# Optimization experiments

Hardware: AMD Instinct MI355X
Metric: run time of the kernel (lower is better)

## Reference

```python
import jax, jax.numpy as jnp
import numpy as np

GROUPS = 256   # == planes (default groups=None -> planes)
NODE_NUM = 32
EPS = 1e-5


def setup_inputs() -> dict:
    key = jax.random.key(0)
    ks = jax.random.split(key, 12)
    b, cin, planes, h, w = 4, 512, 256, 128, 128
    node_fea = planes // NODE_NUM  # 8
    inp = {
        "x": jax.random.normal(ks[0], (b, cin, h, w), jnp.float32),
        "Wt": jax.random.normal(ks[1], (planes, cin), jnp.float32) * 0.02,
        "Wp": jax.random.normal(ks[2], (planes, cin), jnp.float32) * 0.02,
        "Wg": jax.random.normal(ks[3], (planes, cin), jnp.float32) * 0.02,
        "Wz": jax.random.normal(ks[4], (cin,), jnp.float32) * 0.1,  # grouped 1x1 conv, 1 in-ch per group
        "W_adj": jax.random.normal(ks[5], (NODE_NUM, NODE_NUM), jnp.float32) * 0.1,
        "bn_adj_gamma": jnp.ones((NODE_NUM,), jnp.float32),
        "bn_adj_beta": jnp.zeros((NODE_NUM,), jnp.float32),
        "bn_adj_mean": jax.random.normal(ks[6], (NODE_NUM,), jnp.float32) * 0.1,
        "bn_adj_var": jax.random.uniform(ks[7], (NODE_NUM,), jnp.float32) + 0.5,
        "W_wg": jax.random.normal(ks[8], (node_fea, node_fea), jnp.float32) * 0.1,
        "bn_wg_gamma": jnp.ones((node_fea,), jnp.float32),
        "bn_wg_beta": jnp.zeros((node_fea,), jnp.float32),
        "bn_wg_mean": jax.random.normal(ks[9], (node_fea,), jnp.float32) * 0.1,
        "bn_wg_var": jax.random.uniform(ks[10], (node_fea,), jnp.float32) + 0.5,
        "gn_gamma": jnp.ones((cin,), jnp.float32),
        "gn_beta": jnp.zeros((cin,), jnp.float32),
    }
    return inp


def _bn1d_eval(z, mean, var, gamma, beta):
    # BatchNorm1d over channel dim 1 of [b, C, L], eval mode (running stats)
    inv = jax.lax.rsqrt(var + EPS)
    return (z - mean[:, None]) * (inv * gamma)[:, None] + beta[:, None]


def reference(x, Wt, Wp, Wg, Wz, W_adj, bn_adj_gamma, bn_adj_beta, bn_adj_mean,
              bn_adj_var, W_wg, bn_wg_gamma, bn_wg_beta, bn_wg_mean, bn_wg_var,
              gn_gamma, gn_beta):
    b, cin, h, w = x.shape
    # 1x1 convs t/p/g
    t = jnp.einsum('bihw,oi->bohw', x, Wt)
    p = jnp.einsum('bihw,oi->bohw', x, Wp)
    g = jnp.einsum('bihw,oi->bohw', x, Wg)
    planes = t.shape[1]
    node_fea = planes // NODE_NUM
    # per-group dot-product kernel: replaces the Python loop of tiny bmms.
    # _c = planes // GROUPS channels per group; att[b, gidx] = sum(p_g * g_g)
    att = jnp.sum((p * g).reshape(b, GROUPS, -1), axis=-1)  # [b, groups]
    # split(dim=1, node_num) + cat(dim=2): z_idt[b, i, k] = att[b, k*node_num + i]
    z_idt = att.reshape(b, GROUPS // NODE_NUM, NODE_NUM).transpose(0, 2, 1)  # [b, node_num, node_fea]
    # node-adjacency conv (Conv1d k=1 over node dim) + BN + ReLU + residual
    z = jnp.einsum('nm,bmf->bnf', W_adj, z_idt)
    z = _bn1d_eval(z, bn_adj_mean, bn_adj_var, bn_adj_gamma, bn_adj_beta)
    z = jax.nn.relu(z) + z_idt
    # feature conv on transposed layout + BN + ReLU
    z = z.transpose(0, 2, 1)  # [b, node_fea, node_num]
    z = jnp.einsum('fe,ben->bfn', W_wg, z)
    z = _bn1d_eval(z, bn_wg_mean, bn_wg_var, bn_wg_gamma, bn_wg_beta)
    z = jax.nn.relu(z).transpose(0, 2, 1)  # [b, node_num, node_fea]
    # reshape to per-channel scalars and gate t
    zvec = z.reshape(b, planes)[:, :, None, None]  # [b, planes, 1, 1]
    xg = zvec * t  # [b, planes, h, w]
    # grouped 1x1 conv z: groups=planes, 1 input ch / group, r=cin//planes out ch / group
    r = cin // planes
    y = Wz[None, :, None, None] * jnp.repeat(xg, r, axis=1)  # [b, cin, h, w]
    # GroupNorm(num_groups=GROUPS, num_channels=cin)
    yg = y.reshape(b, GROUPS, -1)  # each group: (cin//GROUPS)*h*w elements
    mean = yg.mean(axis=-1, keepdims=True)
    var = yg.var(axis=-1, keepdims=True)
    yn = ((yg - mean) * jax.lax.rsqrt(var + EPS)).reshape(b, cin, h, w)
    yn = yn * gn_gamma[None, :, None, None] + gn_beta[None, :, None, None]
    return yn + x
```

## Files before the change

### kernel.cpp

```cpp
#include <hip/hip_runtime.h>

#define HW 16384
#define CIN 512
#define PL 256
#define EPSF 1e-5f
#define SLO 0.0009765625f

using half8  = __attribute__((ext_vector_type(8))) _Float16;
using half4v = __attribute__((ext_vector_type(4))) _Float16;
using f32x4  = __attribute__((ext_vector_type(4))) float;

__device__ inline void gload_lds16(const void* g, void* l) {
  __builtin_amdgcn_global_load_lds((const __attribute__((address_space(1))) void*)g,
                                   (__attribute__((address_space(3))) void*)l, 16, 0, 0);
}

__global__ __launch_bounds__(256) void k_conv(const float* __restrict__ x,
                                              _Float16* __restrict__ Xh,
                                              _Float16* __restrict__ Xl,
                                              float* __restrict__ xsum) {
  __shared__ float ws4[4];
  int row = blockIdx.x;
  int tid = threadIdx.x;
  const float* xr = x + ((size_t)row << 14);
  _Float16* hr = Xh + ((size_t)row << 14);
  _Float16* lr = Xl + ((size_t)row << 14);
  float s = 0.f;
#pragma unroll
  for (int j = 0; j < 8; ++j) {
    int o = j * 2048 + tid * 8;
    float4 v0 = *reinterpret_cast<const float4*>(xr + o);
    float4 v1 = *reinterpret_cast<const float4*>(xr + o + 4);
    half8 h, l;
    h[0] = (_Float16)v0.x; h[1] = (_Float16)v0.y; h[2] = (_Float16)v0.z; h[3] = (_Float16)v0.w;
    h[4] = (_Float16)v1.x; h[5] = (_Float16)v1.y; h[6] = (_Float16)v1.z; h[7] = (_Float16)v1.w;
    l[0] = (_Float16)((v0.x - (float)h[0]) * 1024.f);
    l[1] = (_Float16)((v0.y - (float)h[1]) * 1024.f);
    l[2] = (_Float16)((v0.z - (float)h[2]) * 1024.f);
    l[3] = (_Float16)((v0.w - (float)h[3]) * 1024.f);
    l[4] = (_Float16)((v1.x - (float)h[4]) * 1024.f);
    l[5] = (_Float16)((v1.y - (float)h[5]) * 1024.f);
    l[6] = (_Float16)((v1.z - (float)h[6]) * 1024.f);
    l[7] = (_Float16)((v1.w - (float)h[7]) * 1024.f);
    *reinterpret_cast<half8*>(hr + o) = h;
    *reinterpret_cast<half8*>(lr + o) = l;
    s += v0.x + v0.y + v0.z + v0.w + v1.x + v1.y + v1.z + v1.w;
  }
#pragma unroll
  for (int m = 1; m < 64; m <<= 1) s += __shfl_xor(s, m);
  if ((tid & 63) == 0) ws4[tid >> 6] = s;
  __syncthreads();
  if (tid == 0) xsum[row] = ws4[0] + ws4[1] + ws4[2] + ws4[3];
}

__global__ __launch_bounds__(256, 4) void k_gx(const _Float16* __restrict__ Xh,
                                               const _Float16* __restrict__ Xl,
                                               float* __restrict__ GH,
                                               float* __restrict__ C1,
                                               _Float16* __restrict__ xT) {
  __shared__ char smem[32768];
  int tid = threadIdx.x;

  if (blockIdx.x < 832) {
    _Float16* lA = (_Float16*)smem;
    _Float16* lB = (_Float16*)(smem + 16384);
    int wg = blockIdx.x;
    int id = (wg & 7) * 104 + (wg >> 3);
    int b = id / 208;
    int rem = id % 208;
    int ks = rem / 26;
    int u = rem % 26;
    int chain, ti, tj;
    if (u < 10) {
      chain = 0;
      ti = 0;
      while ((ti + 1) * (ti + 2) / 2 <= u) ++ti;
      tj = u - ti * (ti + 1) / 2;
    } else {
      chain = 1;
      int t = u - 10;
      ti = t >> 2; tj = t & 3;
    }
    int wave = tid >> 6, lane = tid & 63, l15 = lane & 15, l4 = lane >> 4;
    int wr = wave >> 1, wc = wave & 1;
    const _Float16* Asrc = (chain ? Xl : Xh) + (size_t)b * CIN * HW;
    const _Float16* Bsrc = Xh + (size_t)b * CIN * HW;
    float* D = chain ? C1 : GH;

    int srow = lane >> 3;
    int sgran = (lane & 7) ^ (srow & 7);
    int kbase = ks << 11;
    const _Float16* gA[4];
    const _Float16* gB[4];
#pragma unroll
    for (int i = 0; i < 4; ++i) {
      int row = i * 32 + wave * 8 + srow;
      gA[i] = Asrc + (size_t)(ti * 128 + row) * HW + kbase + sgran * 8;
      gB[i] = Bsrc + (size_t)(tj * 128 + row) * HW + kbase + sgran * 8;
    }
    char* ldA = (char*)lA + wave * 1024;
    char* ldB = (char*)lB + wave * 1024;

    int adA[4][2], adB[4][2];
#pragma unroll
    for (int rf = 0; rf < 4; ++rf) {
      int r = wr * 64 + rf * 16 + l15;
#pragma unroll
      for (int ksub = 0; ksub < 2; ++ksub)
        adA[rf][ksub] = r * 128 + (((ksub * 4 + l4) ^ (r & 7)) << 4);
    }
#pragma unroll
    for (int cf = 0; cf < 4; ++cf) {
      int c = wc * 64 + cf * 16 + l15;
#pragma unroll
      for (int ksub = 0; ksub < 2; ++ksub)
        adB[cf][ksub] = c * 128 + (((ksub * 4 + l4) ^ (c & 7)) << 4);
    }

    f32x4 acc[4][4];
#pragma unroll
    for (int rf = 0; rf < 4; ++rf)
#pragma unroll
      for (int cf = 0; cf < 4; ++cf) acc[rf][cf] = f32x4{0.f, 0.f, 0.f, 0.f};

    for (int s = 0; s < 32; ++s) {
      int ko = s * 64;
#pragma unroll
      for (int i = 0; i < 4; ++i) {
        gload_lds16(gA[i] + ko, ldA + i * 4096);
        gload_lds16(gB[i] + ko, ldB + i * 4096);
      }
      __syncthreads();
#pragma unroll
      for (int ksub = 0; ksub < 2; ++ksub) {
        half8 af[4], bf[4];
#pragma unroll
        for (int rf = 0; rf < 4; ++rf)
          af[rf] = *reinterpret_cast<const half8*>((char*)lA + adA[rf][ksub]);
#pragma unroll
        for (int cf = 0; cf < 4; ++cf)
          bf[cf] = *reinterpret_cast<const half8*>((char*)lB + adB[cf][ksub]);
#pragma unroll
        for (int rf = 0; rf < 4; ++rf)
#pragma unroll
          for (int cf = 0; cf < 4; ++cf)
            acc[rf][cf] = __builtin_amdgcn_mfma_f32_16x16x32_f16(af[rf], bf[cf], acc[rf][cf], 0, 0, 0);
      }
      __syncthreads();
    }

    size_t bo = (size_t)b << 18;
#pragma unroll
    for (int rf = 0; rf < 4; ++rf)
#pragma unroll
      for (int cf = 0; cf < 4; ++cf)
#pragma unroll
        for (int r = 0; r < 4; ++r) {
          int i = ti * 128 + wr * 64 + rf * 16 + l4 * 4 + r;
          int j = tj * 128 + wc * 64 + cf * 16 + l15;
          atomicAdd(D + bo + ((size_t)i << 9) + j, acc[rf][cf][r]);
        }
  } else {
    _Float16* lds = (_Float16*)smem;
    int bid = blockIdx.x - 832;
    int hw0 = (bid & 255) << 6;
    int c0 = ((bid >> 8) & 7) << 6;
    int b = bid >> 11;
    int rl = tid >> 3, seg = tid & 7;
    const _Float16* hb = Xh + ((size_t)b << 23);
#pragma unroll
    for (int pass = 0; pass < 2; ++pass) {
      int cl = pass * 32 + rl;
      half8 v = *reinterpret_cast<const half8*>(hb + ((size_t)(c0 + cl) << 14) + hw0 + seg * 8);
#pragma unroll
      for (int e = 0; e < 8; ++e) lds[(seg * 8 + e) * 72 + cl] = v[e];
    }
    __syncthreads();
    _Float16* tb = xT + (((size_t)b << 14) + hw0) * CIN + c0;
#pragma unroll
    for (int pass = 0; pass < 2; ++pass) {
      int hwl = pass * 32 + rl;
      half8 o = *reinterpret_cast<const half8*>(&lds[hwl * 72 + seg * 8]);
      *reinterpret_cast<half8*>(tb + (size_t)hwl * CIN + seg * 8) = o;
    }
  }
}

__global__ __launch_bounds__(256) void k_sym(const float* __restrict__ GH,
                                             const float* __restrict__ C1,
                                             float* __restrict__ Gs) {
  __shared__ float T1[64 * 65];
  __shared__ float TG[64 * 65];
  int I = blockIdx.x, J = blockIdx.y, b = blockIdx.z;
  int i0 = I << 6, j0 = J << 6;
  bool upper = (I >> 1) >= (J >> 1);
  size_t bo = (size_t)b << 18;
  int tid = threadIdx.x;
  int r = tid >> 2, cs = (tid & 3) << 4;
#pragma unroll
  for (int u = 0; u < 16; u += 4) {
    size_t toff = bo + (((size_t)(j0 + r)) << 9) + i0 + cs + u;
    float4 v = *reinterpret_cast<const float4*>(C1 + toff);
    T1[r * 65 + cs + u + 0] = v.x; T1[r * 65 + cs + u + 1] = v.y;
    T1[r * 65 + cs + u + 2] = v.z; T1[r * 65 + cs + u + 3] = v.w;
    if (!upper) {
      float4 g = *reinterpret_cast<const float4*>(GH + toff);
      TG[r * 65 + cs + u + 0] = g.x; TG[r * 65 + cs + u + 1] = g.y;
      TG[r * 65 + cs + u + 2] = g.z; TG[r * 65 + cs + u + 3] = g.w;
    }
  }
  __syncthreads();
#pragma unroll
  for (int u = 0; u < 16; u += 4) {
    size_t off = bo + (((size_t)(i0 + r)) << 9) + j0 + cs + u;
    float4 c = *reinterpret_cast<const float4*>(C1 + off);
    float t0 = T1[(cs + u + 0) * 65 + r];
    float t1 = T1[(cs + u + 1) * 65 + r];
    float t2 = T1[(cs + u + 2) * 65 + r];
    float t3 = T1[(cs + u + 3) * 65 + r];
    float4 o;
    if (upper) {
      float4 h = *reinterpret_cast<const float4*>(GH + off);
      o.x = h.x + SLO * (c.x + t0);
      o.y = h.y + SLO * (c.y + t1);
      o.z = h.z + SLO * (c.z + t2);
      o.w = h.w + SLO * (c.w + t3);
    } else {
      o.x = TG[(cs + u + 0) * 65 + r] + SLO * (c.x + t0);
      o.y = TG[(cs + u + 1) * 65 + r] + SLO * (c.y + t1);
      o.z = TG[(cs + u + 2) * 65 + r] + SLO * (c.z + t2);
      o.w = TG[(cs + u + 3) * 65 + r] + SLO * (c.w + t3);
    }
    *reinterpret_cast<float4*>(Gs + off) = o;
  }
}

__global__ __launch_bounds__(256) void k_V(const float* __restrict__ Gs,
                                           const float* __restrict__ Wg,
                                           const float* __restrict__ Wt,
                                           float* __restrict__ V) {
  __shared__ float Gl[64 * 65];
  __shared__ float Wl[64 * 65];
  int it = blockIdx.x, ot = blockIdx.y, b = blockIdx.z;
  int i0 = it << 6, o0 = ot << 6;
  int tid = threadIdx.x;
  int srow = tid >> 2, sseg = (tid & 3) << 4;
  const float* gsb = Gs + ((size_t)b << 18);
  int orow = o0 + srow;
  const float* wrow = (orow < 256) ? (Wg + (size_t)orow * 512) : (Wt + (size_t)(orow - 256) * 512);
  float acc[4][4];
#pragma unroll
  for (int a = 0; a < 4; ++a)
#pragma unroll
    for (int c = 0; c < 4; ++c) acc[a][c] = 0.f;
  int oy = (tid >> 4) << 2, ix = (tid & 15) << 2;
  for (int jc = 0; jc < 512; jc += 64) {
    __syncthreads();
#pragma unroll
    for (int u = 0; u < 16; u += 4) {
      float4 g = *reinterpret_cast<const float4*>(gsb + ((size_t)(i0 + srow) << 9) + jc + sseg + u);
      float4 w = *reinterpret_cast<const float4*>(wrow + jc + sseg + u);
      Gl[srow * 65 + sseg + u + 0] = g.x; Gl[srow * 65 + sseg + u + 1] = g.y;
      Gl[srow * 65 + sseg + u + 2] = g.z; Gl[srow * 65 + sseg + u + 3] = g.w;
      Wl[srow * 65 + sseg + u + 0] = w.x; Wl[srow * 65 + sseg + u + 1] = w.y;
      Wl[srow * 65 + sseg + u + 2] = w.z; Wl[srow * 65 + sseg + u + 3] = w.w;
    }
    __syncthreads();
    for (int j = 0; j < 64; ++j) {
      float w0 = Wl[(oy + 0) * 65 + j], w1 = Wl[(oy + 1) * 65 + j];
      float w2 = Wl[(oy + 2) * 65 + j], w3 = Wl[(oy + 3) * 65 + j];
      float g0 = Gl[(ix + 0) * 65 + j], g1 = Gl[(ix + 1) * 65 + j];
      float g2 = Gl[(ix + 2) * 65 + j], g3 = Gl[(ix + 3) * 65 + j];
      acc[0][0] += w0 * g0; acc[0][1] += w0 * g1; acc[0][2] += w0 * g2; acc[0][3] += w0 * g3;
      acc[1][0] += w1 * g0; acc[1][1] += w1 * g1; acc[1][2] += w1 * g2; acc[1][3] += w1 * g3;
      acc[2][0] += w2 * g0; acc[2][1] += w2 * g1; acc[2][2] += w2 * g2; acc[2][3] += w2 * g3;
      acc[3][0] += w3 * g0; acc[3][1] += w3 * g1; acc[3][2] += w3 * g2; acc[3][3] += w3 * g3;
    }
  }
  float* vb = V + ((size_t)b << 18);
#pragma unroll
  for (int a = 0; a < 4; ++a) {
    float4 vv = {acc[a][0], acc[a][1], acc[a][2], acc[a][3]};
    *reinterpret_cast<float4*>(vb + ((size_t)(o0 + oy + a) << 9) + i0 + ix) = vv;
  }
}

__global__ __launch_bounds__(256) void k_red2(const float* __restrict__ V,
                                              const float* __restrict__ xsum,
                                              const float* __restrict__ Wp,
                                              const float* __restrict__ Wt,
                                              float* __restrict__ att,
                                              float* __restrict__ tsum,
                                              float* __restrict__ tsq) {
  int blk = blockIdx.x;
  int b = blk >> 4;
  int og = (blk & 15) << 4;
  int tid = threadIdx.x;
  int ol = tid >> 4, seg = tid & 15;
  int o = og + ol;
  const float* vg = V + ((size_t)b << 18) + ((size_t)o << 9) + seg * 32;
  const float* vt = V + ((size_t)b << 18) + ((size_t)(256 + o) << 9) + seg * 32;
  const float* wp = Wp + (size_t)o * 512 + seg * 32;
  const float* wt = Wt + (size_t)o * 512 + seg * 32;
  const float* xs = xsum + b * CIN + seg * 32;
  float sa = 0.f, sq = 0.f, sm = 0.f;
#pragma unroll
  for (int i = 0; i < 32; i += 4) {
    float4 a = *reinterpret_cast<const float4*>(vg + i);
    float4 p = *reinterpret_cast<const float4*>(wp + i);
    float4 c = *reinterpret_cast<const float4*>(vt + i);
    float4 t = *reinterpret_cast<const float4*>(wt + i);
    float4 s = *reinterpret_cast<const float4*>(xs + i);
    sa += a.x * p.x + a.y * p.y + a.z * p.z + a.w * p.w;
    sq += c.x * t.x + c.y * t.y + c.z * t.z + c.w * t.w;
    sm += t.x * s.x + t.y * s.y + t.z * s.z + t.w * s.w;
  }
#pragma unroll
  for (int m = 1; m < 16; m <<= 1) {
    sa += __shfl_xor(sa, m);
    sq += __shfl_xor(sq, m);
    sm += __shfl_xor(sm, m);
  }
  if (seg == 0) {
    att[b * PL + o] = sa;
    tsq[b * PL + o] = sq;
    tsum[b * PL + o] = sm;
  }
}

__global__ __launch_bounds__(1024) void k_graph(
    const float* __restrict__ att, const float* __restrict__ tsum, const float* __restrict__ tsq,
    const float* __restrict__ W_adj, const float* __restrict__ bnag, const float* __restrict__ bnab,
    const float* __restrict__ bnam, const float* __restrict__ bnav,
    const float* __restrict__ W_wg, const float* __restrict__ bwgg, const float* __restrict__ bwgb,
    const float* __restrict__ bwgm, const float* __restrict__ bwgv,
    const float* __restrict__ Wz, const float* __restrict__ gng, const float* __restrict__ gnb,
    float* __restrict__ sA, float* __restrict__ sB) {
  __shared__ float att_l[4 * 256];
  __shared__ float z_l[4 * 256];
  __shared__ float zv_l[4 * 256];
  int tid = threadIdx.x;
  att_l[tid] = att[tid];
  __syncthreads();
  int b = tid >> 8, r = tid & 255, i = r >> 3, k = r & 7;
  float z1 = 0.f;
#pragma unroll
  for (int m = 0; m < 32; ++m) z1 += W_adj[i * 32 + m] * att_l[b * 256 + k * 32 + m];
  float inv = rsqrtf(bnav[i] + EPSF);
  float z = (z1 - bnam[i]) * inv * bnag[i] + bnab[i];
  z = fmaxf(z, 0.f) + att_l[b * 256 + k * 32 + i];
  z_l[b * 256 + i * 8 + k] = z;
  __syncthreads();
  float z2 = 0.f;
#pragma unroll
  for (int e = 0; e < 8; ++e) z2 += W_wg[k * 8 + e] * z_l[b * 256 + i * 8 + e];
  float inv2 = rsqrtf(bwgv[k] + EPSF);
  z2 = (z2 - bwgm[k]) * inv2 * bwgg[k] + bwgb[k];
  zv_l[b * 256 + i * 8 + k] = fmaxf(z2, 0.f);
  __syncthreads();
  int g = r;
  float s = zv_l[b * 256 + g];
  float m1 = tsum[b * 256 + g] * (1.f / 16384.f);
  float m2 = tsq[b * 256 + g] * (1.f / 16384.f);
  float a0 = Wz[2 * g] * s, a1 = Wz[2 * g + 1] * s;
  float mu = 0.5f * (a0 + a1) * m1;
  float ey2 = 0.5f * (a0 * a0 + a1 * a1) * m2;
  float var = ey2 - mu * mu;
  float invg = rsqrtf(var + EPSF);
  int c = b * CIN + 2 * g;
  sA[c]     = a0 * invg * gng[2 * g];
  sA[c + 1] = a1 * invg * gng[2 * g + 1];
  sB[c]     = gnb[2 * g]     - mu * invg * gng[2 * g];
  sB[c + 1] = gnb[2 * g + 1] - mu * invg * gng[2 * g + 1];
}

__global__ __launch_bounds__(256) void k_M(const float* __restrict__ Wt,
                                           const float* __restrict__ sA,
                                           _Float16* __restrict__ M) {
  int idx = blockIdx.x * 256 + threadIdx.x;
  int k8 = idx & 63;
  int c = (idx >> 6) & 511;
  int b = idx >> 15;
  float s = sA[b * 512 + c];
  const float* wrow = Wt + ((size_t)(c >> 1) << 9) + k8 * 8;
  int kbase = k8 * 8;
  half8 h;
#pragma unroll
  for (int j = 0; j < 8; ++j) {
    float v = s * wrow[j] + ((kbase + j) == c ? 1.f : 0.f);
    h[j] = (_Float16)v;
  }
  *reinterpret_cast<half8*>(M + (((size_t)(b * 512 + c)) << 9) + kbase) = h;
}

__global__ __launch_bounds__(256, 4) void k_tout(const _Float16* __restrict__ xT,
                                                 const _Float16* __restrict__ M,
                                                 const float* __restrict__ sB,
                                                 float* __restrict__ out) {
  __shared__ _Float16 lA[128 * 32];
  __shared__ _Float16 lB[128 * 32];
  int wg = blockIdx.x;
  int id = (wg & 7) * 256 + (wg >> 3);
  int b = id >> 9;
  int rem = id & 511;
  int ct = rem >> 7;
  int ht = rem & 127;
  int tid = threadIdx.x;
  int wave = tid >> 6, lane = tid & 63, l15 = lane & 15, l4 = lane >> 4;
  int wr = wave >> 1, wc = wave & 1;
  const _Float16* Mb = M + ((size_t)b << 18);
  const _Float16* xTb = xT + (size_t)b * HW * CIN;

  int srow = lane >> 2;
  int gran = (lane & 3) ^ ((srow >> 1) & 3);
  const _Float16* gA[2];
  const _Float16* gB[2];
#pragma unroll
  for (int i = 0; i < 2; ++i) {
    int row = i * 64 + wave * 16 + srow;
    gA[i] = Mb + ((size_t)(ct * 128 + row) << 9) + gran * 8;
    gB[i] = xTb + ((size_t)(ht * 128 + row) << 9) + gran * 8;
  }
  char* ldA = (char*)lA + wave * 1024;
  char* ldB = (char*)lB + wave * 1024;

  int adA[4], adB[4];
#pragma unroll
  for (int rf = 0; rf < 4; ++rf) {
    int r = wr * 64 + rf * 16 + l15;
    adA[rf] = r * 64 + ((l4 ^ ((r >> 1) & 3)) << 4);
  }
#pragma unroll
  for (int cf = 0; cf < 4; ++cf) {
    int c = wc * 64 + cf * 16 + l15;
    adB[cf] = c * 64 + ((l4 ^ ((c >> 1) & 3)) << 4);
  }

  f32x4 acc[4][4];
#pragma unroll
  for (int rf = 0; rf < 4; ++rf)
#pragma unroll
    for (int cf = 0; cf < 4; ++cf) acc[rf][cf] = f32x4{0.f, 0.f, 0.f, 0.f};

  for (int s = 0; s < 16; ++s) {
    int ko = s * 32;
    gload_lds16(gA[0] + ko, ldA);
    gload_lds16(gA[1] + ko, ldA + 4096);
    gload_lds16(gB[0] + ko, ldB);
    gload_lds16(gB[1] + ko, ldB + 4096);
    __syncthreads();
    half8 af[4], bf[4];
#pragma unroll
    for (int rf = 0; rf < 4; ++rf) af[rf] = *reinterpret_cast<const half8*>((char*)lA + adA[rf]);
#pragma unroll
    for (int cf = 0; cf < 4; ++cf) bf[cf] = *reinterpret_cast<const half8*>((char*)lB + adB[cf]);
#pragma unroll
    for (int rf = 0; rf < 4; ++rf)
#pragma unroll
      for (int cf = 0; cf < 4; ++cf)
        acc[rf][cf] = __builtin_amdgcn_mfma_f32_16x16x32_f16(af[rf], bf[cf], acc[rf][cf], 0, 0, 0);
    __syncthreads();
  }

  size_t outb = ((size_t)b * CIN) << 14;
#pragma unroll
  for (int rf = 0; rf < 4; ++rf) {
#pragma unroll
    for (int r = 0; r < 4; ++r) {
      int c = ct * 128 + wr * 64 + rf * 16 + l4 * 4 + r;
      float bb = sB[b * CIN + c];
      size_t off = outb + ((size_t)c << 14) + ht * 128 + wc * 64 + l15;
#pragma unroll
      for (int cf = 0; cf < 4; ++cf)
        out[off + cf * 16] = acc[rf][cf][r] + bb;
    }
  }
}

extern "C" void kernel_launch(void* const* d_in, const int* in_sizes, int n_in,
                              void* d_out, int out_size, void* d_ws, size_t ws_size,
                              hipStream_t stream) {
  const float* x    = (const float*)d_in[0];
  const float* Wt   = (const float*)d_in[1];
  const float* Wp   = (const float*)d_in[2];
  const float* Wg   = (const float*)d_in[3];
  const float* Wz   = (const float*)d_in[4];
  const float* Wadj = (const float*)d_in[5];
  const float* bnag = (const float*)d_in[6];
  const float* bnab = (const float*)d_in[7];
  const float* bnam = (const float*)d_in[8];
  const float* bnav = (const float*)d_in[9];
  const float* Wwg  = (const float*)d_in[10];
  const float* bwgg = (const float*)d_in[11];
  const float* bwgb = (const float*)d_in[12];
  const float* bwgm = (const float*)d_in[13];
  const float* bwgv = (const float*)d_in[14];
  const float* gng  = (const float*)d_in[15];
  const float* gnb  = (const float*)d_in[16];

  char* ws = (char*)d_ws;
  _Float16* xT = (_Float16*)(ws);
  float* GH   = (float*)(ws + 67371008);
  float* C1   = (float*)(ws + 71565312);
  float* Gs   = (float*)(ws + 75759616);
  float* V    = (float*)(ws + 79953920);
  float* xsum = (float*)(ws + 84148224);
  float* att  = (float*)(ws + 84156416);
  float* tsum = (float*)(ws + 84160512);
  float* tsq  = (float*)(ws + 84164608);
  float* sA   = (float*)(ws + 84168704);
  float* sB   = (float*)(ws + 84176896);
  if (ws_size < (size_t)84185088) return;
  _Float16* M = (_Float16*)GH;

  _Float16* Xh = (_Float16*)((char*)d_out);
  _Float16* Xl = (_Float16*)((char*)d_out + 67108864);
  float* out = (float*)d_out;

  hipMemsetAsync(GH, 0, 8388608, stream);
  k_conv<<<dim3(2048), dim3(256), 0, stream>>>(x, Xh, Xl, xsum);
  k_gx<<<dim3(9024), dim3(256), 0, stream>>>(Xh, Xl, GH, C1, xT);
  k_sym<<<dim3(8, 8, 4), dim3(256), 0, stream>>>(GH, C1, Gs);
  k_V<<<dim3(8, 8, 4), dim3(256), 0, stream>>>(Gs, Wg, Wt, V);
  k_red2<<<dim3(64), dim3(256), 0, stream>>>(V, xsum, Wp, Wt, att, tsum, tsq);
  k_graph<<<dim3(1), dim3(1024), 0, stream>>>(att, tsum, tsq, Wadj, bnag, bnab, bnam, bnav,
                                              Wwg, bwgg, bwgb, bwgm, bwgv, Wz, gng, gnb, sA, sB);
  k_M<<<dim3(512), dim3(256), 0, stream>>>(Wt, sA, M);
  k_tout<<<dim3(2048), dim3(256), 0, stream>>>(xT, M, sB, out);
}
```

Measured before the change: 263.4 us.

## Double K-step depth in k_tout GEMM and swizzle LDS transpose writes

The k_tout GEMM now stages a 64-wide K slice per iteration instead of 32. That halves the number of main-loop iterations and barrier pairs, and the LDS swizzle is reworked to an 8-granule XOR pattern. Separately, the xT transpose path in the conv kernel XOR-swizzles its LDS layout to reduce bank conflicts on scattered half writes. The costs are doubled LDS per block for k_tout, which may lower occupancy under the 4-blocks launch bound, and more address arithmetic.

```diff
diff --git a/kernel.cpp b/kernel.cpp
--- a/kernel.cpp
+++ b/kernel.cpp
@@ -171,16 +171,21 @@
 #pragma unroll
     for (int pass = 0; pass < 2; ++pass) {
       int cl = pass * 32 + rl;
+      int chunk = cl >> 3, wi = cl & 7;
       half8 v = *reinterpret_cast<const half8*>(hb + ((size_t)(c0 + cl) << 14) + hw0 + seg * 8);
 #pragma unroll
-      for (int e = 0; e < 8; ++e) lds[(seg * 8 + e) * 72 + cl] = v[e];
+      for (int e = 0; e < 8; ++e) {
+        int r = seg * 8 + e;
+        lds[r * 72 + ((chunk ^ ((r >> 3) & 7)) << 3) + wi] = v[e];
+      }
     }
     __syncthreads();
     _Float16* tb = xT + (((size_t)b << 14) + hw0) * CIN + c0;
 #pragma unroll
     for (int pass = 0; pass < 2; ++pass) {
       int hwl = pass * 32 + rl;
-      half8 o = *reinterpret_cast<const half8*>(&lds[hwl * 72 + seg * 8]);
+      int chp = seg ^ ((hwl >> 3) & 7);
+      half8 o = *reinterpret_cast<const half8*>(&lds[hwl * 72 + (chp << 3)]);
       *reinterpret_cast<half8*>(tb + (size_t)hwl * CIN + seg * 8) = o;
     }
   }
@@ -397,8 +402,8 @@
                                                  const _Float16* __restrict__ M,
                                                  const float* __restrict__ sB,
                                                  float* __restrict__ out) {
-  __shared__ _Float16 lA[128 * 32];
-  __shared__ _Float16 lB[128 * 32];
+  __shared__ _Float16 lA[128 * 64];
+  __shared__ _Float16 lB[128 * 64];
   int wg = blockIdx.x;
   int id = (wg & 7) * 256 + (wg >> 3);
   int b = id >> 9;
@@ -411,29 +416,33 @@
   const _Float16* Mb = M + ((size_t)b << 18);
   const _Float16* xTb = xT + (size_t)b * HW * CIN;
 
-  int srow = lane >> 2;
-  int gran = (lane & 3) ^ ((srow >> 1) & 3);
-  const _Float16* gA[2];
-  const _Float16* gB[2];
-#pragma unroll
-  for (int i = 0; i < 2; ++i) {
-    int row = i * 64 + wave * 16 + srow;
-    gA[i] = Mb + ((size_t)(ct * 128 + row) << 9) + gran * 8;
-    gB[i] = xTb + ((size_t)(ht * 128 + row) << 9) + gran * 8;
+  int srow = lane >> 3;
+  int sgran = (lane & 7) ^ (srow & 7);
+  const _Float16* gA[4];
+  const _Float16* gB[4];
+#pragma unroll
+  for (int i = 0; i < 4; ++i) {
+    int row = i * 32 + wave * 8 + srow;
+    gA[i] = Mb + ((size_t)(ct * 128 + row) << 9) + sgran * 8;
+    gB[i] = xTb + ((size_t)(ht * 128 + row) << 9) + sgran * 8;
   }
   char* ldA = (char*)lA + wave * 1024;
   char* ldB = (char*)lB + wave * 1024;
 
-  int adA[4], adB[4];
+  int adA[4][2], adB[4][2];
 #pragma unroll
   for (int rf = 0; rf < 4; ++rf) {
     int r = wr * 64 + rf * 16 + l15;
-    adA[rf] = r * 64 + ((l4 ^ ((r >> 1) & 3)) << 4);
+#pragma unroll
+    for (int ksub = 0; ksub < 2; ++ksub)
+      adA[rf][ksub] = r * 128 + (((ksub * 4 + l4) ^ (r & 7)) << 4);
   }
 #pragma unroll
   for (int cf = 0; cf < 4; ++cf) {
     int c = wc * 64 + cf * 16 + l15;
-    adB[cf] = c * 64 + ((l4 ^ ((c >> 1) & 3)) << 4);
+#pragma unroll
+    for (int ksub = 0; ksub < 2; ++ksub)
+      adB[cf][ksub] = c * 128 + (((ksub * 4 + l4) ^ (c & 7)) << 4);
   }
 
   f32x4 acc[4][4];
@@ -442,23 +451,29 @@
 #pragma unroll
     for (int cf = 0; cf < 4; ++cf) acc[rf][cf] = f32x4{0.f, 0.f, 0.f, 0.f};
 
-  for (int s = 0; s < 16; ++s) {
-    int ko = s * 32;
-    gload_lds16(gA[0] + ko, ldA);
-    gload_lds16(gA[1] + ko, ldA + 4096);
-    gload_lds16(gB[0] + ko, ldB);
-    gload_lds16(gB[1] + ko, ldB + 4096);
+  for (int s = 0; s < 8; ++s) {
+    int ko = s * 64;
+#pragma unroll
+    for (int i = 0; i < 4; ++i) {
+      gload_lds16(gA[i] + ko, ldA + i * 4096);
+      gload_lds16(gB[i] + ko, ldB + i * 4096);
+    }
     __syncthreads();
-    half8 af[4], bf[4];
-#pragma unroll
-    for (int rf = 0; rf < 4; ++rf) af[rf] = *reinterpret_cast<const half8*>((char*)lA + adA[rf]);
-#pragma unroll
-    for (int cf = 0; cf < 4; ++cf) bf[cf] = *reinterpret_cast<const half8*>((char*)lB + adB[cf]);
-#pragma unroll
-    for (int rf = 0; rf < 4; ++rf)
+#pragma unroll
+    for (int ksub = 0; ksub < 2; ++ksub) {
+      half8 af[4], bf[4];
+#pragma unroll
+      for (int rf = 0; rf < 4; ++rf)
+        af[rf] = *reinterpret_cast<const half8*>((char*)lA + adA[rf][ksub]);
 #pragma unroll
       for (int cf = 0; cf < 4; ++cf)
-        acc[rf][cf] = __builtin_amdgcn_mfma_f32_16x16x32_f16(af[rf], bf[cf], acc[rf][cf], 0, 0, 0);
+        bf[cf] = *reinterpret_cast<const half8*>((char*)lB + adB[cf][ksub]);
+#pragma unroll
+      for (int rf = 0; rf < 4; ++rf)
+#pragma unroll
+        for (int cf = 0; cf < 4; ++cf)
+          acc[rf][cf] = __builtin_amdgcn_mfma_f32_16x16x32_f16(af[rf], bf[cf], acc[rf][cf], 0, 0, 0);
+    }
     __syncthreads();
   }
 
```

After: 263.6 us, median of 2. Within noise of the previous version (+0.0%).
